# Kernel optimization log

Measured on AMD Instinct MI355X. Metric: run time of the kernel, lower is better.

## Reference

```python
import jax, jax.numpy as jnp
import numpy as np


def setup_inputs() -> dict:
    key = jax.random.key(0)
    X = jax.random.normal(key, (8, 64, 64, 64), dtype=jnp.float32)
    return {"X": X}


def reference(X):
    N, C, h, w = X.shape
    x1 = X.reshape(N, C, h * w)            # [N, C, HW]
    x2 = jnp.transpose(x1, (0, 2, 1))      # [N, HW, C]
    scores = jnp.einsum('bnc,bcm->bnm', x2, x1)  # [N, HW, HW]
    c = jax.nn.softmax(scores, axis=2)
    out = jnp.einsum('bnm,bmc->bnc', c, x2)      # [N, HW, C]
    out = jnp.transpose(out, (0, 2, 1)).reshape(N, C, h, w)
    return out
```

## Files before the change

kernel.cpp:

```cpp
#include <hip/hip_runtime.h>
#include <math.h>
#include <type_traits>


#define SEQ 4096
#define DIM 64
#define LDB 72
#define LDO 68
#define QSCALE 1.2011224087864498f

typedef __attribute__((ext_vector_type(8))) short  short8;
typedef __attribute__((ext_vector_type(4))) float  f32x4;

__device__ __forceinline__ unsigned short f2bf(float f) {
    union { float f; unsigned int u; } x; x.f = f;
    unsigned int u = x.u + 0x7FFFu + ((x.u >> 16) & 1u);
    return (unsigned short)(u >> 16);
}
__device__ __forceinline__ float bf2f(unsigned short h) {
    union { unsigned int u; float f; } x; x.u = ((unsigned int)h) << 16; return x.f;
}

#define LDT 68
__global__ __launch_bounds__(256) void prepass3(const float* __restrict__ X,
                                                unsigned short* __restrict__ Xbf,
                                                unsigned short* __restrict__ XbfT,
                                                float* __restrict__ Norms,
                                                float* __restrict__ MaxPart) {
    __shared__ __align__(16) unsigned short sT[64 * LDT];
    __shared__ float sRed[4];
    const int b = blockIdx.y, m0 = blockIdx.x * 64;
    const float* Xb = X + (size_t)b * DIM * SEQ;
    unsigned short* Bb = Xbf  + (size_t)b * DIM * SEQ;
    unsigned short* Tb = XbfT + (size_t)b * SEQ * DIM;
    const int t = threadIdx.x, w = t >> 6;
    const int mw = t & 15, cg = t >> 4;

    #pragma unroll
    for (int cr = 0; cr < 4; ++cr) {
        const int c = cg * 4 + cr;
        const f32x4 v = *(const f32x4*)(Xb + (size_t)c * SEQ + m0 + 4 * mw);
        *(ushort4*)(Bb + (size_t)c * SEQ + m0 + 4 * mw) =
            make_ushort4(f2bf(v.x), f2bf(v.y), f2bf(v.z), f2bf(v.w));
        sT[(4 * mw + 0) * LDT + c] = f2bf(v.x * QSCALE);
        sT[(4 * mw + 1) * LDT + c] = f2bf(v.y * QSCALE);
        sT[(4 * mw + 2) * LDT + c] = f2bf(v.z * QSCALE);
        sT[(4 * mw + 3) * LDT + c] = f2bf(v.w * QSCALE);
    }
    __syncthreads();
    const int m = t >> 2, ck = t & 3;
    const short8 a0 = *(const short8*)(sT + m * LDT + ck * 16);
    const short8 a1 = *(const short8*)(sT + m * LDT + ck * 16 + 8);
    *(short8*)(Tb + (size_t)(m0 + m) * DIM + ck * 16)     = a0;
    *(short8*)(Tb + (size_t)(m0 + m) * DIM + ck * 16 + 8) = a1;
    float s = 0.f;
    #pragma unroll
    for (int i = 0; i < 8; ++i) {
        const float f0 = bf2f((unsigned short)a0[i]);
        const float f1 = bf2f((unsigned short)a1[i]);
        s += f0 * f0 + f1 * f1;
    }
    s += __shfl_xor(s, 1);
    s += __shfl_xor(s, 2);
    const float nm = sqrtf(s);
    if (ck == 0) Norms[(size_t)b * SEQ + m0 + m] = nm;
    float mx = nm;
    #pragma unroll
    for (int d = 4; d < 64; d <<= 1) mx = fmaxf(mx, __shfl_xor(mx, d));
    if ((t & 63) == 0) sRed[w] = mx;
    __syncthreads();
    if (t == 0)
        MaxPart[b * 64 + blockIdx.x] =
            fmaxf(fmaxf(sRed[0], sRed[1]), fmaxf(sRed[2], sRed[3]));
}

template <bool PARTIAL>
__global__ __launch_bounds__(128, 2) void attn_split(const unsigned short* __restrict__ Xbf,
                                                     const unsigned short* __restrict__ XbfT,
                                                     const float* __restrict__ Norms,
                                                     const float* __restrict__ MaxPart,
                                                     float* __restrict__ Obase,
                                                     float* __restrict__ Lbase,
                                                     int niter) {
    __shared__ __align__(16) unsigned char smem[40960];
    unsigned short* sK = (unsigned short*)smem;
    unsigned short* sV = (unsigned short*)(smem + 16384);
    unsigned short* sP = (unsigned short*)(smem + 32768);
    float*          sO = (float*)smem;

    const int tid  = threadIdx.x;
    const int lane = tid & 63;
    const int w    = tid >> 6;
    const int l15  = lane & 15;
    const int quad = lane >> 4;

    const int b   = blockIdx.y;
    const int s0  = blockIdx.x * 64;
    const int h   = blockIdx.z;
    const int kt0 = h * niter;
    const unsigned short* Bb = Xbf  + (size_t)b * DIM * SEQ;
    const unsigned short* Tb = XbfT + (size_t)b * SEQ * DIM;
    float* Optr = Obase + (size_t)h * 8 * DIM * SEQ;
    float* Lptr = PARTIAL ? (Lbase + (size_t)h * 8 * SEQ) : nullptr;

    float mxn = MaxPart[b * 64 + lane];
    #pragma unroll
    for (int d = 1; d < 64; d <<= 1) mxn = fmaxf(mxn, __shfl_xor(mxn, d));

    short8 qf[2][2];
    f32x4 cin[2];
    #pragma unroll
    for (int qt = 0; qt < 2; ++qt) {
        const int row = s0 + 32 * w + 16 * qt + l15;
        const unsigned short* qp = Tb + (size_t)row * DIM + quad * 8;
        qf[qt][0] = *(const short8*)(qp);
        qf[qt][1] = *(const short8*)(qp + 32);
        const float mrow = Norms[(size_t)b * SEQ + row] * mxn;
        cin[qt] = (f32x4){-mrow, -mrow, -mrow, -mrow};
    }

    f32x4 acc_o[2][4];
    #pragma unroll
    for (int qt = 0; qt < 2; ++qt)
        #pragma unroll
        for (int ct = 0; ct < 4; ++ct) acc_o[qt][ct] = (f32x4){0.f, 0.f, 0.f, 0.f};
    float lp[2] = {0.f, 0.f};

    const int rsw = l15 & 7;
    const unsigned short* kb[2];
    const unsigned short* vb[2];
    #pragma unroll
    for (int ks = 0; ks < 2; ++ks) {
        const int cgr = (((quad + 4 * ks) ^ rsw) << 3);
        kb[ks] = sK + (l15 << 6) + cgr;
        vb[ks] = sV + (l15 << 6) + cgr;
    }
    unsigned short* const sProw = sP + w * 32 * 64 + (l15 << 6);
    unsigned short* pw[4];
    #pragma unroll
    for (int mt = 0; mt < 4; ++mt)
        pw[mt] = sProw + ((((2 * mt + (quad >> 1)) ^ rsw) << 3) + ((quad & 1) << 2));
    const unsigned short* pr[2];
    #pragma unroll
    for (int ks = 0; ks < 2; ++ks)
        pr[ks] = sProw + (((quad + 4 * ks) ^ rsw) << 3);

    const int rl = lane >> 3, cgs = (lane & 7) ^ rl;
    const unsigned short* gK[4];
    const unsigned short* gV[4];
    #pragma unroll
    for (int j = 0; j < 4; ++j) {
        const int row_j = w * 8 + j * 16 + rl;
        gK[j] = Tb + (size_t)kt0 * 4096 + row_j * 64 + cgs * 8;
        gV[j] = Bb + (size_t)row_j * 4096 + (size_t)kt0 * 64 + cgs * 8;
    }
    auto stageTo = [&](auto HC) {
        constexpr int HALF = decltype(HC)::value;
        #pragma unroll
        for (int j = 0; j < 4; ++j) {
            __builtin_amdgcn_global_load_lds(
                (const __attribute__((address_space(1))) unsigned int*)gK[j],
                (__attribute__((address_space(3))) unsigned int*)(sK + HALF * 4096 + (w * 8 + j * 16) * 64),
                16, 0, 0);
            __builtin_amdgcn_global_load_lds(
                (const __attribute__((address_space(1))) unsigned int*)gV[j],
                (__attribute__((address_space(3))) unsigned int*)(sV + HALF * 4096 + (w * 8 + j * 16) * 64),
                16, 0, 0);
        }
        #pragma unroll
        for (int j = 0; j < 4; ++j) { gK[j] += 4096; gV[j] += 64; }
    };

    auto computeT = [&](auto HC) {
        constexpr int HALF = decltype(HC)::value;
        short8 kf[2][4], vf[2][4];
        #pragma unroll
        for (int t4 = 0; t4 < 4; ++t4)
            #pragma unroll
            for (int ks = 0; ks < 2; ++ks) {
                kf[ks][t4] = *(const short8*)(kb[ks] + HALF * 4096 + t4 * 1024);
                vf[ks][t4] = *(const short8*)(vb[ks] + HALF * 4096 + t4 * 1024);
            }
        #pragma unroll
        for (int qt = 0; qt < 2; ++qt) {
            #pragma unroll
            for (int mt = 0; mt < 4; ++mt) {
                f32x4 a = cin[qt];
                a = __builtin_amdgcn_mfma_f32_16x16x32_bf16(kf[0][mt], qf[qt][0], a, 0, 0, 0);
                a = __builtin_amdgcn_mfma_f32_16x16x32_bf16(kf[1][mt], qf[qt][1], a, 0, 0, 0);
                const float p0 = exp2f(a[0]);
                const float p1 = exp2f(a[1]);
                const float p2 = exp2f(a[2]);
                const float p3 = exp2f(a[3]);
                lp[qt] += (p0 + p1) + (p2 + p3);
                const unsigned u0 = __float_as_uint(p0) + 0x8000u;
                const unsigned u1 = __float_as_uint(p1) + 0x8000u;
                const unsigned u2 = __float_as_uint(p2) + 0x8000u;
                const unsigned u3 = __float_as_uint(p3) + 0x8000u;
                const unsigned lo = __builtin_amdgcn_perm(u1, u0, 0x07060302u);
                const unsigned hi = __builtin_amdgcn_perm(u3, u2, 0x07060302u);
                *(uint2*)(pw[mt] + qt * 1024) = make_uint2(lo, hi);
            }
            const short8 pf0 = *(const short8*)(pr[0] + qt * 1024);
            const short8 pf1 = *(const short8*)(pr[1] + qt * 1024);
            #pragma unroll
            for (int ct = 0; ct < 4; ++ct) {
                acc_o[qt][ct] = __builtin_amdgcn_mfma_f32_16x16x32_bf16(pf0, vf[0][ct], acc_o[qt][ct], 0, 0, 0);
                acc_o[qt][ct] = __builtin_amdgcn_mfma_f32_16x16x32_bf16(pf1, vf[1][ct], acc_o[qt][ct], 0, 0, 0);
            }
        }
    };

    std::integral_constant<int, 0> H0;
    std::integral_constant<int, 1> H1;

    stageTo(H0);
    __syncthreads();
    for (int it = 0; it < niter; it += 2) {
        if (it + 1 < niter) stageTo(H1);
        computeT(H0);
        __syncthreads();
        if (it + 2 < niter) stageTo(H0);
        computeT(H1);
        __syncthreads();
    }

    #pragma unroll
    for (int qt = 0; qt < 2; ++qt) {
        lp[qt] += __shfl_xor(lp[qt], 16);
        lp[qt] += __shfl_xor(lp[qt], 32);
    }

    if (PARTIAL) {
        if (quad == 0) {
            #pragma unroll
            for (int qt = 0; qt < 2; ++qt)
                Lptr[(size_t)b * SEQ + s0 + 32 * w + 16 * qt + l15] = lp[qt];
        }
    } else {
        #pragma unroll
        for (int qt = 0; qt < 2; ++qt) {
            float inv[4];
            #pragma unroll
            for (int r = 0; r < 4; ++r) inv[r] = 1.f / __shfl(lp[qt], 4 * quad + r);
            #pragma unroll
            for (int ct = 0; ct < 4; ++ct)
                #pragma unroll
                for (int r = 0; r < 4; ++r) acc_o[qt][ct][r] *= inv[r];
        }
    }

    #pragma unroll
    for (int qt = 0; qt < 2; ++qt)
        #pragma unroll
        for (int ct = 0; ct < 4; ++ct) {
            const int c = 16 * ct + l15;
            #pragma unroll
            for (int r = 0; r < 4; ++r)
                sO[c * LDO + 32 * w + 16 * qt + 4 * quad + r] = acc_o[qt][ct][r];
        }
    __syncthreads();
    const int mw = tid & 15, cg = tid >> 4;
    #pragma unroll
    for (int cc = 0; cc < 8; ++cc) {
        const int c = cg + 8 * cc;
        const f32x4 v = *(const f32x4*)(sO + c * LDO + 4 * mw);
        *(f32x4*)(Optr + ((size_t)b * DIM + c) * SEQ + s0 + 4 * mw) = v;
    }
}

__global__ __launch_bounds__(256) void combine_kernel(const float* __restrict__ O0,
                                                      const float* __restrict__ O1,
                                                      const float* __restrict__ L0,
                                                      const float* __restrict__ L1,
                                                      float* __restrict__ Out) {
    const int gid = blockIdx.x * 256 + threadIdx.x;
    const size_t base = (size_t)gid * 4;
    const int s = (int)(base & 4095);
    const int b = (int)(base >> 18);
    const f32x4 o0 = *(const f32x4*)(O0 + base);
    const f32x4 o1 = *(const f32x4*)(O1 + base);
    const f32x4 l0 = *(const f32x4*)(L0 + b * SEQ + s);
    const f32x4 l1 = *(const f32x4*)(L1 + b * SEQ + s);
    f32x4 o;
    #pragma unroll
    for (int i = 0; i < 4; ++i) o[i] = (o0[i] + o1[i]) / (l0[i] + l1[i]);
    *(f32x4*)(Out + base) = o;
}

__global__ __launch_bounds__(256, 2) void attn_fallback(const float* __restrict__ X,
                                                        float* __restrict__ Out) {
    __shared__ __align__(16) unsigned char smem[27648];
    unsigned short* sK = (unsigned short*)smem;
    unsigned short* sV = (unsigned short*)(smem + 9216);
    unsigned short* sP = (unsigned short*)(smem + 18432);
    float*          sO = (float*)smem;
    const int tid  = threadIdx.x;
    const int lane = tid & 63;
    const int w    = tid >> 6;
    const int l15  = lane & 15;
    const int quad = lane >> 4;
    const int b  = blockIdx.y;
    const int s0 = blockIdx.x * 64;
    const float* Xb = X + (size_t)b * DIM * SEQ;
    const int mgrp = tid & 15;
    const int c0   = tid >> 4;

    for (int cc = 0; cc < 4; ++cc) {
        int c = c0 + 16 * cc;
        const f32x4 v = *(const f32x4*)(Xb + (size_t)c * SEQ + s0 + 4 * mgrp);
        sK[(4 * mgrp + 0) * LDB + c] = f2bf(v.x);
        sK[(4 * mgrp + 1) * LDB + c] = f2bf(v.y);
        sK[(4 * mgrp + 2) * LDB + c] = f2bf(v.z);
        sK[(4 * mgrp + 3) * LDB + c] = f2bf(v.w);
    }
    __syncthreads();
    short8 qf0, qf1;
    {
        const int row = 16 * w + l15;
        qf0 = *(const short8*)(sK + row * LDB + quad * 8);
        qf1 = *(const short8*)(sK + row * LDB + 32 + quad * 8);
    }
    __syncthreads();
    f32x4 acc_o[4];
    for (int ct = 0; ct < 4; ++ct) acc_o[ct] = (f32x4){0.f, 0.f, 0.f, 0.f};
    float m_i[4] = {-1e30f, -1e30f, -1e30f, -1e30f};
    float l_i[4] = {0.f, 0.f, 0.f, 0.f};
    for (int kt = 0; kt < SEQ / 64; ++kt) {
        const int m0 = kt * 64;
        for (int cc = 0; cc < 4; ++cc) {
            int c = c0 + 16 * cc;
            const f32x4 v = *(const f32x4*)(Xb + (size_t)c * SEQ + m0 + 4 * mgrp);
            unsigned short h0 = f2bf(v.x), h1 = f2bf(v.y), h2 = f2bf(v.z), h3 = f2bf(v.w);
            *(ushort4*)(sV + c * LDB + 4 * mgrp) = make_ushort4(h0, h1, h2, h3);
            sK[(4 * mgrp + 0) * LDB + c] = h0;
            sK[(4 * mgrp + 1) * LDB + c] = h1;
            sK[(4 * mgrp + 2) * LDB + c] = h2;
            sK[(4 * mgrp + 3) * LDB + c] = h3;
        }
        __syncthreads();
        short8 vf[2][4];
        for (int ks = 0; ks < 2; ++ks)
            for (int ct = 0; ct < 4; ++ct)
                vf[ks][ct] = *(const short8*)(sV + (16 * ct + l15) * LDB + ks * 32 + quad * 8);
        f32x4 acc_s[4];
        for (int mt = 0; mt < 4; ++mt) {
            const int row = 16 * mt + l15;
            const short8 kf0 = *(const short8*)(sK + row * LDB + quad * 8);
            const short8 kf1 = *(const short8*)(sK + row * LDB + 32 + quad * 8);
            f32x4 a = (f32x4){0.f, 0.f, 0.f, 0.f};
            a = __builtin_amdgcn_mfma_f32_16x16x32_bf16(qf0, kf0, a, 0, 0, 0);
            a = __builtin_amdgcn_mfma_f32_16x16x32_bf16(qf1, kf1, a, 0, 0, 0);
            acc_s[mt] = a;
        }
        float alpha[4];
        for (int r = 0; r < 4; ++r) {
            float mx = fmaxf(fmaxf(acc_s[0][r], acc_s[1][r]), fmaxf(acc_s[2][r], acc_s[3][r]));
            mx = fmaxf(mx, __shfl_xor(mx, 1));
            mx = fmaxf(mx, __shfl_xor(mx, 2));
            mx = fmaxf(mx, __shfl_xor(mx, 4));
            mx = fmaxf(mx, __shfl_xor(mx, 8));
            const float mnew = fmaxf(m_i[r], mx);
            alpha[r] = __expf(m_i[r] - mnew);
            m_i[r] = mnew;
        }
        float rowsum[4] = {0.f, 0.f, 0.f, 0.f};
        unsigned short pb[4][4];
        for (int mt = 0; mt < 4; ++mt)
            for (int r = 0; r < 4; ++r) {
                const float p = __expf(acc_s[mt][r] - m_i[r]);
                rowsum[r] += p;
                pb[mt][r] = f2bf(p);
            }
        for (int r = 0; r < 4; ++r) {
            float s = rowsum[r];
            s += __shfl_xor(s, 1);
            s += __shfl_xor(s, 2);
            s += __shfl_xor(s, 4);
            s += __shfl_xor(s, 8);
            l_i[r] = alpha[r] * l_i[r] + s;
        }
        for (int ct = 0; ct < 4; ++ct)
            for (int r = 0; r < 4; ++r)
                acc_o[ct][r] *= alpha[r];
        for (int mt = 0; mt < 4; ++mt)
            for (int r = 0; r < 4; ++r)
                sP[(16 * w + quad * 4 + r) * LDB + l15 + 16 * mt] = pb[mt][r];
        __syncthreads();
        const short8 pf0 = *(const short8*)(sP + (16 * w + l15) * LDB + quad * 8);
        const short8 pf1 = *(const short8*)(sP + (16 * w + l15) * LDB + 32 + quad * 8);
        for (int ct = 0; ct < 4; ++ct) {
            acc_o[ct] = __builtin_amdgcn_mfma_f32_16x16x32_bf16(pf0, vf[0][ct], acc_o[ct], 0, 0, 0);
            acc_o[ct] = __builtin_amdgcn_mfma_f32_16x16x32_bf16(pf1, vf[1][ct], acc_o[ct], 0, 0, 0);
        }
    }
    float inv[4];
    for (int r = 0; r < 4; ++r) inv[r] = 1.f / l_i[r];
    for (int ct = 0; ct < 4; ++ct) {
        const int c = 16 * ct + l15;
        for (int r = 0; r < 4; ++r)
            sO[c * LDO + 16 * w + quad * 4 + r] = acc_o[ct][r] * inv[r];
    }
    __syncthreads();
    for (int cc = 0; cc < 4; ++cc) {
        const int c = c0 + 16 * cc;
        const f32x4 v = *(const f32x4*)(sO + c * LDO + 4 * mgrp);
        *(f32x4*)(Out + (size_t)b * DIM * SEQ + (size_t)c * SEQ + s0 + 4 * mgrp) = v;
    }
}

extern "C" void kernel_launch(void* const* d_in, const int* in_sizes, int n_in,
                              void* d_out, int out_size, void* d_ws, size_t ws_size,
                              hipStream_t stream) {
    const float* X = (const float*)d_in[0];
    float* Out = (float*)d_out;
    const size_t elems = (size_t)8 * SEQ * DIM;
    const size_t offXbfT  = elems * 2;
    const size_t offNorms = offXbfT + elems * 2;
    const size_t offMaxP  = offNorms + (size_t)8 * SEQ * 4;
    const size_t offOpart = offMaxP + 8 * 64 * 4;
    const size_t offLpart = offOpart + 2 * elems * 4;
    const size_t need_split = offLpart + 2 * (size_t)8 * SEQ * 4;
    const size_t need_h1    = offOpart;

    if (ws_size >= need_h1) {
        unsigned short* Xbf   = (unsigned short*)d_ws;
        unsigned short* XbfT  = (unsigned short*)((char*)d_ws + offXbfT);
        float* Norms   = (float*)((char*)d_ws + offNorms);
        float* MaxPart = (float*)((char*)d_ws + offMaxP);
        prepass3<<<dim3(64, 8), 256, 0, stream>>>(X, Xbf, XbfT, Norms, MaxPart);
        if (ws_size >= need_split) {
            float* O0 = (float*)((char*)d_ws + offOpart);
            float* O1 = O0 + elems;
            float* L0 = (float*)((char*)d_ws + offLpart);
            float* L1 = L0 + (size_t)8 * SEQ;
            attn_split<true><<<dim3(64, 8, 2), 128, 0, stream>>>(Xbf, XbfT, Norms, MaxPart,
                                                                 O0, L0, 32);
            const int ngrp = (int)(elems / 4 / 256);
            combine_kernel<<<ngrp, 256, 0, stream>>>(O0, O1, L0, L1, Out);
        } else {
            attn_split<false><<<dim3(64, 8, 1), 128, 0, stream>>>(Xbf, XbfT, Norms, MaxPart,
                                                                  Out, nullptr, 64);
        }
    } else {
        attn_fallback<<<dim3(64, 8), 256, 0, stream>>>(X, Out);
    }
}
```

Measured before the change: 131.3 us.

## Split attention KV range four ways with smaller tiles and bf16 partials

Cuts the key/value tile per iteration from 64 to 32 rows, halving LDS to raise the occupancy hint to 4 blocks per SM, and splits the sequence across 4 partial blocks instead of 2. Partial outputs are written as bf16 to reduce workspace traffic, and a new combine kernel sums the four partials and normalizes. It also drops the round-to-nearest bias when packing P to bf16, truncating instead. The trade-offs are more iterations and barriers per tile, extra combine reads, and lower precision in the partial sums.

```diff
diff --git a/kernel.cpp b/kernel.cpp
--- a/kernel.cpp
+++ b/kernel.cpp
@@ -75,17 +75,18 @@
 }
 
 template <bool PARTIAL>
-__global__ __launch_bounds__(128, 2) void attn_split(const unsigned short* __restrict__ Xbf,
-                                                     const unsigned short* __restrict__ XbfT,
-                                                     const float* __restrict__ Norms,
-                                                     const float* __restrict__ MaxPart,
-                                                     float* __restrict__ Obase,
-                                                     float* __restrict__ Lbase,
-                                                     int niter) {
-    __shared__ __align__(16) unsigned char smem[40960];
+__global__ __launch_bounds__(128, 4) void attn_split4(const unsigned short* __restrict__ Xbf,
+                                                      const unsigned short* __restrict__ XbfT,
+                                                      const float* __restrict__ Norms,
+                                                      const float* __restrict__ MaxPart,
+                                                      unsigned short* __restrict__ Obf,
+                                                      float* __restrict__ Lbase,
+                                                      float* __restrict__ Out,
+                                                      int niter) {
+    __shared__ __align__(16) unsigned char smem[20480];
     unsigned short* sK = (unsigned short*)smem;
-    unsigned short* sV = (unsigned short*)(smem + 16384);
-    unsigned short* sP = (unsigned short*)(smem + 32768);
+    unsigned short* sV = (unsigned short*)(smem + 8192);
+    unsigned short* sP = (unsigned short*)(smem + 16384);
     float*          sO = (float*)smem;
 
     const int tid  = threadIdx.x;
@@ -100,8 +101,6 @@
     const int kt0 = h * niter;
     const unsigned short* Bb = Xbf  + (size_t)b * DIM * SEQ;
     const unsigned short* Tb = XbfT + (size_t)b * SEQ * DIM;
-    float* Optr = Obase + (size_t)h * 8 * DIM * SEQ;
-    float* Lptr = PARTIAL ? (Lbase + (size_t)h * 8 * SEQ) : nullptr;
 
     float mxn = MaxPart[b * 64 + lane];
     #pragma unroll
@@ -126,65 +125,65 @@
         for (int ct = 0; ct < 4; ++ct) acc_o[qt][ct] = (f32x4){0.f, 0.f, 0.f, 0.f};
     float lp[2] = {0.f, 0.f};
 
-    const int rsw = l15 & 7;
+    const int rsw  = l15 & 7;
+    const int vkey = (l15 & 3) ^ (l15 >> 2);
     const unsigned short* kb[2];
-    const unsigned short* vb[2];
-    #pragma unroll
-    for (int ks = 0; ks < 2; ++ks) {
-        const int cgr = (((quad + 4 * ks) ^ rsw) << 3);
-        kb[ks] = sK + (l15 << 6) + cgr;
-        vb[ks] = sV + (l15 << 6) + cgr;
-    }
-    unsigned short* const sProw = sP + w * 32 * 64 + (l15 << 6);
-    unsigned short* pw[4];
-    #pragma unroll
-    for (int mt = 0; mt < 4; ++mt)
-        pw[mt] = sProw + ((((2 * mt + (quad >> 1)) ^ rsw) << 3) + ((quad & 1) << 2));
-    const unsigned short* pr[2];
     #pragma unroll
     for (int ks = 0; ks < 2; ++ks)
-        pr[ks] = sProw + (((quad + 4 * ks) ^ rsw) << 3);
-
-    const int rl = lane >> 3, cgs = (lane & 7) ^ rl;
-    const unsigned short* gK[4];
-    const unsigned short* gV[4];
-    #pragma unroll
-    for (int j = 0; j < 4; ++j) {
-        const int row_j = w * 8 + j * 16 + rl;
-        gK[j] = Tb + (size_t)kt0 * 4096 + row_j * 64 + cgs * 8;
-        gV[j] = Bb + (size_t)row_j * 4096 + (size_t)kt0 * 64 + cgs * 8;
+        kb[ks] = sK + (l15 << 6) + (((quad + 4 * ks) ^ rsw) << 3);
+    const unsigned short* vb = sV + (l15 << 5) + ((quad ^ vkey) << 3);
+    unsigned short* const prow = sP + (w << 10) + (l15 << 5);
+    unsigned short* pw[2];
+    #pragma unroll
+    for (int mt = 0; mt < 2; ++mt)
+        pw[mt] = prow + ((((2 * mt + (quad >> 1)) ^ vkey) << 3) + ((quad & 1) << 2));
+    const unsigned short* pr = prow + ((quad ^ vkey) << 3);
+
+    const int rl8 = lane >> 3, c8 = lane & 7;
+    const int cgsK = c8 ^ rl8;
+    const int rv = lane >> 2, cv = lane & 3;
+    const int cvs = cv ^ ((rv & 3) ^ ((rv >> 2) & 3));
+    const unsigned short* gK[2];
+    const unsigned short* gV[2];
+    #pragma unroll
+    for (int j = 0; j < 2; ++j) {
+        const int rowK = w * 16 + j * 8 + rl8;
+        const int rowV = w * 32 + j * 16 + rv;
+        gK[j] = Tb + (size_t)(kt0 * 32 + rowK) * 64 + cgsK * 8;
+        gV[j] = Bb + (size_t)rowV * 4096 + kt0 * 32 + cvs * 8;
     }
     auto stageTo = [&](auto HC) {
         constexpr int HALF = decltype(HC)::value;
         #pragma unroll
-        for (int j = 0; j < 4; ++j) {
+        for (int j = 0; j < 2; ++j) {
             __builtin_amdgcn_global_load_lds(
                 (const __attribute__((address_space(1))) unsigned int*)gK[j],
-                (__attribute__((address_space(3))) unsigned int*)(sK + HALF * 4096 + (w * 8 + j * 16) * 64),
+                (__attribute__((address_space(3))) unsigned int*)(sK + HALF * 2048 + (w * 16 + j * 8) * 64),
                 16, 0, 0);
             __builtin_amdgcn_global_load_lds(
                 (const __attribute__((address_space(1))) unsigned int*)gV[j],
-                (__attribute__((address_space(3))) unsigned int*)(sV + HALF * 4096 + (w * 8 + j * 16) * 64),
+                (__attribute__((address_space(3))) unsigned int*)(sV + HALF * 2048 + (w * 32 + j * 16) * 32),
                 16, 0, 0);
         }
         #pragma unroll
-        for (int j = 0; j < 4; ++j) { gK[j] += 4096; gV[j] += 64; }
+        for (int j = 0; j < 2; ++j) { gK[j] += 2048; gV[j] += 32; }
     };
 
     auto computeT = [&](auto HC) {
         constexpr int HALF = decltype(HC)::value;
-        short8 kf[2][4], vf[2][4];
-        #pragma unroll
-        for (int t4 = 0; t4 < 4; ++t4)
-            #pragma unroll
-            for (int ks = 0; ks < 2; ++ks) {
-                kf[ks][t4] = *(const short8*)(kb[ks] + HALF * 4096 + t4 * 1024);
-                vf[ks][t4] = *(const short8*)(vb[ks] + HALF * 4096 + t4 * 1024);
-            }
+        short8 kf[2][2], vf[4];
+        #pragma unroll
+        for (int mt = 0; mt < 2; ++mt)
+            #pragma unroll
+            for (int ks = 0; ks < 2; ++ks)
+                kf[ks][mt] = *(const short8*)(kb[ks] + HALF * 2048 + mt * 1024);
+        #pragma unroll
+        for (int ct = 0; ct < 4; ++ct)
+            vf[ct] = *(const short8*)(vb + HALF * 2048 + ct * 512);
         #pragma unroll
         for (int qt = 0; qt < 2; ++qt) {
             #pragma unroll
-            for (int mt = 0; mt < 4; ++mt) {
+            for (int mt = 0; mt < 2; ++mt) {
                 f32x4 a = cin[qt];
                 a = __builtin_amdgcn_mfma_f32_16x16x32_bf16(kf[0][mt], qf[qt][0], a, 0, 0, 0);
                 a = __builtin_amdgcn_mfma_f32_16x16x32_bf16(kf[1][mt], qf[qt][1], a, 0, 0, 0);
@@ -193,21 +192,14 @@
                 const float p2 = exp2f(a[2]);
                 const float p3 = exp2f(a[3]);
                 lp[qt] += (p0 + p1) + (p2 + p3);
-                const unsigned u0 = __float_as_uint(p0) + 0x8000u;
-                const unsigned u1 = __float_as_uint(p1) + 0x8000u;
-                const unsigned u2 = __float_as_uint(p2) + 0x8000u;
-                const unsigned u3 = __float_as_uint(p3) + 0x8000u;
-                const unsigned lo = __builtin_amdgcn_perm(u1, u0, 0x07060302u);
-                const unsigned hi = __builtin_amdgcn_perm(u3, u2, 0x07060302u);
-                *(uint2*)(pw[mt] + qt * 1024) = make_uint2(lo, hi);
+                const unsigned lo = __builtin_amdgcn_perm(__float_as_uint(p1), __float_as_uint(p0), 0x07060302u);
+                const unsigned hi = __builtin_amdgcn_perm(__float_as_uint(p3), __float_as_uint(p2), 0x07060302u);
+                *(uint2*)(pw[mt] + qt * 512) = make_uint2(lo, hi);
             }
-            const short8 pf0 = *(const short8*)(pr[0] + qt * 1024);
-            const short8 pf1 = *(const short8*)(pr[1] + qt * 1024);
-            #pragma unroll
-            for (int ct = 0; ct < 4; ++ct) {
-                acc_o[qt][ct] = __builtin_amdgcn_mfma_f32_16x16x32_bf16(pf0, vf[0][ct], acc_o[qt][ct], 0, 0, 0);
-                acc_o[qt][ct] = __builtin_amdgcn_mfma_f32_16x16x32_bf16(pf1, vf[1][ct], acc_o[qt][ct], 0, 0, 0);
-            }
+            const short8 pf = *(const short8*)(pr + qt * 512);
+            #pragma unroll
+            for (int ct = 0; ct < 4; ++ct)
+                acc_o[qt][ct] = __builtin_amdgcn_mfma_f32_16x16x32_bf16(pf, vf[ct], acc_o[qt][ct], 0, 0, 0);
         }
     };
 
@@ -235,7 +227,7 @@
         if (quad == 0) {
             #pragma unroll
             for (int qt = 0; qt < 2; ++qt)
-                Lptr[(size_t)b * SEQ + s0 + 32 * w + 16 * qt + l15] = lp[qt];
+                (Lbase + (size_t)h * 8 * SEQ)[(size_t)b * SEQ + s0 + 32 * w + 16 * qt + l15] = lp[qt];
         }
     } else {
         #pragma unroll
@@ -261,30 +253,45 @@
         }
     __syncthreads();
     const int mw = tid & 15, cg = tid >> 4;
-    #pragma unroll
-    for (int cc = 0; cc < 8; ++cc) {
-        const int c = cg + 8 * cc;
-        const f32x4 v = *(const f32x4*)(sO + c * LDO + 4 * mw);
-        *(f32x4*)(Optr + ((size_t)b * DIM + c) * SEQ + s0 + 4 * mw) = v;
-    }
-}
-
-__global__ __launch_bounds__(256) void combine_kernel(const float* __restrict__ O0,
-                                                      const float* __restrict__ O1,
-                                                      const float* __restrict__ L0,
-                                                      const float* __restrict__ L1,
-                                                      float* __restrict__ Out) {
+    if (PARTIAL) {
+        unsigned short* Op = Obf + (size_t)h * 8 * DIM * SEQ;
+        #pragma unroll
+        for (int cc = 0; cc < 8; ++cc) {
+            const int c = cg + 8 * cc;
+            const f32x4 v = *(const f32x4*)(sO + c * LDO + 4 * mw);
+            *(ushort4*)(Op + ((size_t)b * DIM + c) * SEQ + s0 + 4 * mw) =
+                make_ushort4(f2bf(v.x), f2bf(v.y), f2bf(v.z), f2bf(v.w));
+        }
+    } else {
+        #pragma unroll
+        for (int cc = 0; cc < 8; ++cc) {
+            const int c = cg + 8 * cc;
+            const f32x4 v = *(const f32x4*)(sO + c * LDO + 4 * mw);
+            *(f32x4*)(Out + ((size_t)b * DIM + c) * SEQ + s0 + 4 * mw) = v;
+        }
+    }
+}
+
+__global__ __launch_bounds__(256) void combine4(const unsigned short* __restrict__ Obf,
+                                                const float* __restrict__ Lp,
+                                                float* __restrict__ Out) {
     const int gid = blockIdx.x * 256 + threadIdx.x;
     const size_t base = (size_t)gid * 4;
     const int s = (int)(base & 4095);
     const int b = (int)(base >> 18);
-    const f32x4 o0 = *(const f32x4*)(O0 + base);
-    const f32x4 o1 = *(const f32x4*)(O1 + base);
-    const f32x4 l0 = *(const f32x4*)(L0 + b * SEQ + s);
-    const f32x4 l1 = *(const f32x4*)(L1 + b * SEQ + s);
+    f32x4 os = (f32x4){0.f, 0.f, 0.f, 0.f};
+    f32x4 ls = (f32x4){0.f, 0.f, 0.f, 0.f};
+    #pragma unroll
+    for (int h = 0; h < 4; ++h) {
+        const ushort4 o = *(const ushort4*)(Obf + (size_t)h * 2097152 + base);
+        os[0] += bf2f(o.x); os[1] += bf2f(o.y); os[2] += bf2f(o.z); os[3] += bf2f(o.w);
+        const f32x4 l = *(const f32x4*)(Lp + (size_t)h * 8 * SEQ + b * SEQ + s);
+        #pragma unroll
+        for (int i = 0; i < 4; ++i) ls[i] += l[i];
+    }
     f32x4 o;
     #pragma unroll
-    for (int i = 0; i < 4; ++i) o[i] = (o0[i] + o1[i]) / (l0[i] + l1[i]);
+    for (int i = 0; i < 4; ++i) o[i] = os[i] / ls[i];
     *(f32x4*)(Out + base) = o;
 }
 
@@ -418,10 +425,10 @@
     const size_t offXbfT  = elems * 2;
     const size_t offNorms = offXbfT + elems * 2;
     const size_t offMaxP  = offNorms + (size_t)8 * SEQ * 4;
-    const size_t offOpart = offMaxP + 8 * 64 * 4;
-    const size_t offLpart = offOpart + 2 * elems * 4;
-    const size_t need_split = offLpart + 2 * (size_t)8 * SEQ * 4;
-    const size_t need_h1    = offOpart;
+    const size_t offObf   = offMaxP + 8 * 64 * 4;
+    const size_t offLpart = offObf + 4 * elems * 2;
+    const size_t need_split = offLpart + 4 * (size_t)8 * SEQ * 4;
+    const size_t need_h1    = offObf;
 
     if (ws_size >= need_h1) {
         unsigned short* Xbf   = (unsigned short*)d_ws;
@@ -430,17 +437,14 @@
         float* MaxPart = (float*)((char*)d_ws + offMaxP);
         prepass3<<<dim3(64, 8), 256, 0, stream>>>(X, Xbf, XbfT, Norms, MaxPart);
         if (ws_size >= need_split) {
-            float* O0 = (float*)((char*)d_ws + offOpart);
-            float* O1 = O0 + elems;
-            float* L0 = (float*)((char*)d_ws + offLpart);
-            float* L1 = L0 + (size_t)8 * SEQ;
-            attn_split<true><<<dim3(64, 8, 2), 128, 0, stream>>>(Xbf, XbfT, Norms, MaxPart,
-                                                                 O0, L0, 32);
-            const int ngrp = (int)(elems / 4 / 256);
-            combine_kernel<<<ngrp, 256, 0, stream>>>(O0, O1, L0, L1, Out);
+            unsigned short* Obf = (unsigned short*)((char*)d_ws + offObf);
+            float* Lp = (float*)((char*)d_ws + offLpart);
+            attn_split4<true><<<dim3(64, 8, 4), 128, 0, stream>>>(Xbf, XbfT, Norms, MaxPart,
+                                                                  Obf, Lp, nullptr, 32);
+            combine4<<<(int)(elems / 1024), 256, 0, stream>>>(Obf, Lp, Out);
         } else {
-            attn_split<false><<<dim3(64, 8, 1), 128, 0, stream>>>(Xbf, XbfT, Norms, MaxPart,
-                                                                  Out, nullptr, 64);
+            attn_split4<false><<<dim3(64, 8, 1), 128, 0, stream>>>(Xbf, XbfT, Norms, MaxPart,
+                                                                   nullptr, nullptr, Out, 128);
         }
     } else {
         attn_fallback<<<dim3(64, 8), 256, 0, stream>>>(X, Out);
```

Result: no change. 128.8 us (-1.9%).
